# Optimization experiments

Hardware: AMD Instinct MI355X
Metric: run time of the kernel (lower is better)

The kernel has to match this reference:

```python
import jax, jax.numpy as jnp
import numpy as np

N, S, E, HEADS = 8, 2048, 1024, 16


def setup_inputs() -> dict:
    root = jax.random.key(0)
    k1, k2, k3, k4, k5, k6 = jax.random.split(root, 6)
    query = jax.random.normal(k1, (N, S, E), jnp.float32)
    key_t = jax.random.normal(k2, (N, S, E), jnp.float32)
    value = jax.random.normal(k3, (N, S, E), jnp.float32)
    # mask broadcasts against the (buggy) energy tensor of shape (N, S, H, H)
    mask = jax.random.randint(k4, (1, 1, HEADS, HEADS), 0, 2, jnp.int32)
    # guarantee no all-masked softmax row (avoid NaN)
    diag = jnp.arange(HEADS)
    mask = mask.at[0, 0, diag, diag].set(1)
    W_out = jax.random.normal(k5, (E, E), jnp.float32) / np.float32(np.sqrt(E))
    b_out = jax.random.normal(k6, (E,), jnp.float32) * 0.02
    return {"query": query, "key": key_t, "value": value, "mask": mask,
            "W_out": W_out, "b_out": b_out, "heads": HEADS}


def reference(query, key, value, mask, W_out, b_out, heads):
    # Faithful translation of the original forward, INCLUDING its einsum-label
    # bug: tensors are transposed to (N, H, S, D) but the einsum subscripts
    # treat axis 1 as 'q/k' and axis 2 as 'h', so softmax runs over heads.
    n, q_len, e = query.shape
    d = e // heads
    inv_scale = np.float32(1.0 / np.sqrt(d))
    q = query.reshape(n, q_len, heads, d).transpose(0, 2, 1, 3)   # (N,H,S,D)
    k = key.reshape(n, q_len, heads, d).transpose(0, 2, 1, 3)     # (N,H,S,D)
    v = value.reshape(n, q_len, heads, d).transpose(0, 2, 1, 3)   # (N,H,S,D)
    # labels applied to transposed tensors -> energy shape (N, S, H, H)
    energy = jnp.einsum('nqhd,nkhd->nhqk', q, k) * inv_scale
    energy = jnp.where(mask == 0, -jnp.inf, energy)
    attention = jax.nn.softmax(energy, axis=-1)                   # over heads axis
    out = jnp.einsum('nhql,nlhd->nqhd', attention, v)             # (N,H,S,D)
    out = out.reshape(n, q_len, e)                                # raw memory reinterp, as torch does
    return out @ W_out.T + b_out
```

## Files before the change

### kernel.cpp

```cpp
#include <hip/hip_runtime.h>
#include <stdint.h>

#define S_LEN 2048
#define EMB 1024

typedef __bf16 bf16x8 __attribute__((ext_vector_type(8)));
typedef float f32x4 __attribute__((ext_vector_type(4)));

__device__ __forceinline__ unsigned short f2bf(float f) {
  unsigned int b = __float_as_uint(f);
  b += 0x7FFFu + ((b >> 16) & 1u);
  return (unsigned short)(b >> 16);
}

__device__ __forceinline__ bf16x8 cvt8(float4 a, float4 b) {
  bf16x8 r;
  r[0] = (__bf16)a.x; r[1] = (__bf16)a.y; r[2] = (__bf16)a.z; r[3] = (__bf16)a.w;
  r[4] = (__bf16)b.x; r[5] = (__bf16)b.y; r[6] = (__bf16)b.z; r[7] = (__bf16)b.w;
  return r;
}

#define GLD16(gp, lp)                                                          \
  __builtin_amdgcn_global_load_lds(                                            \
      (const __attribute__((address_space(1))) void*)(gp),                     \
      (__attribute__((address_space(3))) void*)(lp), 16, 0, 0)

__global__ __launch_bounds__(256) void attn_kernel(
    const float* __restrict__ Q, const float* __restrict__ K,
    const float* __restrict__ V, const int* __restrict__ mask,
    __bf16* __restrict__ X) {
  __shared__ __bf16 Vt[4][64][24];
  __shared__ __bf16 As[4][16][24];

  const int lane = threadIdx.x & 63;
  const int wv = threadIdx.x >> 6;
  const int pos = blockIdx.x * 4 + wv;
  const int n = pos >> 11;
  const int s = pos & 2047;
  const int j16 = lane & 15;
  const int grp = lane >> 4;

  const float* qrow = Q + (size_t)pos * EMB;
  const float* krow = K + (size_t)pos * EMB;
  const float* vrow = V + (size_t)pos * EMB;

#pragma unroll
  for (int c = 0; c < 4; ++c) {
    const int e = c * 256 + lane * 4;
    const float4 vv = *(const float4*)(vrow + e);
    const int hi = e >> 6;
    const int d0 = e & 63;
    Vt[wv][d0 + 0][hi] = (__bf16)vv.x;
    Vt[wv][d0 + 1][hi] = (__bf16)vv.y;
    Vt[wv][d0 + 2][hi] = (__bf16)vv.z;
    Vt[wv][d0 + 3][hi] = (__bf16)vv.w;
  }

  const int fo = j16 * 64 + grp * 8;
  bf16x8 qa[2], kb[2];
#pragma unroll
  for (int t = 0; t < 2; ++t) {
    float4 a0 = *(const float4*)(qrow + fo + t * 32);
    float4 a1 = *(const float4*)(qrow + fo + t * 32 + 4);
    float4 b0 = *(const float4*)(krow + fo + t * 32);
    float4 b1 = *(const float4*)(krow + fo + t * 32 + 4);
    qa[t] = cvt8(a0, a1);
    kb[t] = cvt8(b0, b1);
  }

  f32x4 en = {0.f, 0.f, 0.f, 0.f};
  en = __builtin_amdgcn_mfma_f32_16x16x32_bf16(qa[0], kb[0], en, 0, 0, 0);
  en = __builtin_amdgcn_mfma_f32_16x16x32_bf16(qa[1], kb[1], en, 0, 0, 0);

  float p[4];
#pragma unroll
  for (int r = 0; r < 4; ++r) {
    const int i = grp * 4 + r;
    float g = en[r] * 0.125f;
    if (mask[i * 16 + j16] == 0) g = -1e30f;
    p[r] = g;
  }
#pragma unroll
  for (int off = 1; off < 16; off <<= 1) {
#pragma unroll
    for (int r = 0; r < 4; ++r) {
      float o = __shfl_xor(p[r], off);
      (void)o;
    }
  }
  float mx[4], ex[4], sm[4];
#pragma unroll
  for (int r = 0; r < 4; ++r) mx[r] = p[r];
#pragma unroll
  for (int off = 1; off < 16; off <<= 1)
#pragma unroll
    for (int r = 0; r < 4; ++r) mx[r] = fmaxf(mx[r], __shfl_xor(mx[r], off));
#pragma unroll
  for (int r = 0; r < 4; ++r) {
    ex[r] = __expf(p[r] - mx[r]);
    sm[r] = ex[r];
  }
#pragma unroll
  for (int off = 1; off < 16; off <<= 1)
#pragma unroll
    for (int r = 0; r < 4; ++r) sm[r] += __shfl_xor(sm[r], off);
#pragma unroll
  for (int r = 0; r < 4; ++r) {
    const float inv = __builtin_amdgcn_rcpf(sm[r]);
    As[wv][grp * 4 + r][j16] = (__bf16)(ex[r] * inv);
  }

  bf16x8 af;
#pragma unroll
  for (int e = 0; e < 8; ++e) af[e] = (__bf16)0.f;
  if (grp < 2) af = *(const bf16x8*)&As[wv][j16][grp * 8];

  const size_t xbase =
      ((size_t)n * S_LEN + (s >> 4)) * EMB + (size_t)((s & 15) * 64);
  __bf16* xp = X + xbase + j16 + (size_t)grp * 4 * 128 * EMB;
#pragma unroll
  for (int c = 0; c < 4; ++c) {
    bf16x8 bv;
#pragma unroll
    for (int e = 0; e < 8; ++e) bv[e] = (__bf16)0.f;
    if (grp < 2) bv = *(const bf16x8*)&Vt[wv][c * 16 + j16][grp * 8];
    f32x4 o = {0.f, 0.f, 0.f, 0.f};
    o = __builtin_amdgcn_mfma_f32_16x16x32_bf16(af, bv, o, 0, 0, 0);
#pragma unroll
    for (int r = 0; r < 4; ++r)
      xp[(size_t)r * 128 * EMB + c * 16] = (__bf16)o[r];
  }
}

__global__ __launch_bounds__(256) void wconv_kernel(
    const float* __restrict__ W, unsigned short* __restrict__ Wb) {
  const int idx = blockIdx.x * 256 + threadIdx.x;
  float4 w = *(const float4*)(W + (size_t)idx * 4);
  ushort4 o;
  o.x = f2bf(w.x);
  o.y = f2bf(w.y);
  o.z = f2bf(w.z);
  o.w = f2bf(w.w);
  *(ushort4*)(Wb + (size_t)idx * 4) = o;
}

__global__ __launch_bounds__(256) void gemm_kernel(
    const unsigned short* __restrict__ A, const unsigned short* __restrict__ B,
    const float* __restrict__ bias, float* __restrict__ C) {
  __shared__ unsigned short sA[128 * 32];
  __shared__ unsigned short sB[128 * 32];

  int bid = blockIdx.x;
  const int cpx = gridDim.x >> 3;
  bid = (bid & 7) * cpx + (bid >> 3);
  const int tileM = (bid >> 3) * 128;
  const int tileN = (bid & 7) * 128;

  const int t = threadIdx.x;
  const int lane = t & 63;
  const int wid = t >> 6;
  const int wm = wid >> 1, wn = wid & 1;
  const int lrow = lane & 15;
  const int lgrp = lane >> 4;

  f32x4 acc[4][4];
#pragma unroll
  for (int a = 0; a < 4; ++a)
#pragma unroll
    for (int b = 0; b < 4; ++b) acc[a][b] = (f32x4){0.f, 0.f, 0.f, 0.f};

  const int row0 = t >> 2;
  const int kk = (t & 3) * 8;
  const size_t abase = ((size_t)(tileM + row0)) * 1024 + kk;
  const size_t bbase = ((size_t)(tileN + row0)) * 1024 + kk;

  for (int k0 = 0; k0 < 1024; k0 += 32) {
#pragma unroll
    for (int c = 0; c < 2; ++c) {
      GLD16(A + abase + (size_t)c * 64 * 1024 + k0,
            (char*)sA + c * 4096 + t * 16);
      GLD16(B + bbase + (size_t)c * 64 * 1024 + k0,
            (char*)sB + c * 4096 + t * 16);
    }
    __syncthreads();

    bf16x8 af[4], bfr[4];
#pragma unroll
    for (int mi = 0; mi < 4; ++mi)
      af[mi] = *(const bf16x8*)&sA[(wm * 64 + mi * 16 + lrow) * 32 + lgrp * 8];
#pragma unroll
    for (int ni = 0; ni < 4; ++ni)
      bfr[ni] = *(const bf16x8*)&sB[(wn * 64 + ni * 16 + lrow) * 32 + lgrp * 8];
#pragma unroll
    for (int mi = 0; mi < 4; ++mi)
#pragma unroll
      for (int ni = 0; ni < 4; ++ni)
        acc[mi][ni] = __builtin_amdgcn_mfma_f32_16x16x32_bf16(
            af[mi], bfr[ni], acc[mi][ni], 0, 0, 0);
    __syncthreads();
  }

#pragma unroll
  for (int ni = 0; ni < 4; ++ni) {
    const int col = tileN + wn * 64 + ni * 16 + lrow;
    const float bv = bias[col];
#pragma unroll
    for (int mi = 0; mi < 4; ++mi) {
      const int row = tileM + wm * 64 + mi * 16 + lgrp * 4;
#pragma unroll
      for (int r = 0; r < 4; ++r)
        C[(size_t)(row + r) * 1024 + col] = acc[mi][ni][r] + bv;
    }
  }
}

extern "C" void kernel_launch(void* const* d_in, const int* in_sizes, int n_in,
                              void* d_out, int out_size, void* d_ws,
                              size_t ws_size, hipStream_t stream) {
  const float* Q = (const float*)d_in[0];
  const float* K = (const float*)d_in[1];
  const float* V = (const float*)d_in[2];
  const int* mask = (const int*)d_in[3];
  const float* W = (const float*)d_in[4];
  const float* bias = (const float*)d_in[5];
  float* out = (float*)d_out;

  __bf16* X = (__bf16*)d_ws;
  unsigned short* Wb =
      (unsigned short*)((char*)d_ws + (size_t)32 * 1024 * 1024);

  hipLaunchKernelGGL(attn_kernel, dim3(8 * S_LEN / 4), dim3(256), 0, stream, Q,
                     K, V, mask, X);
  hipLaunchKernelGGL(wconv_kernel, dim3(1024), dim3(256), 0, stream, W, Wb);
  hipLaunchKernelGGL(gemm_kernel, dim3(1024), dim3(256), 0, stream,
                     (const unsigned short*)X, Wb, bias, out);
}
```

Before: 99.15 us.

## Transpose MFMA operands in attention kernel to drop LDS V staging and shuffles

Swaps the MFMA operand order so each lane holds one query row's four energies across lane groups. The softmax reduction then needs only two cross-group shuffles, and the mask is read as a single int4. V is read straight from global memory into MFMA fragments, which removes the LDS transpose buffer. Outputs are written as packed bf16x4 stores instead of scattered scalar stores. The cost is strided scalar global loads of V, 8 per fragment, which may coalesce worse than the old float4 loads.

```diff
diff --git a/kernel.cpp b/kernel.cpp
--- a/kernel.cpp
+++ b/kernel.cpp
@@ -5,6 +5,7 @@
 #define EMB 1024
 
 typedef __bf16 bf16x8 __attribute__((ext_vector_type(8)));
+typedef __bf16 bf16x4 __attribute__((ext_vector_type(4)));
 typedef float f32x4 __attribute__((ext_vector_type(4)));
 
 __device__ __forceinline__ unsigned short f2bf(float f) {
@@ -29,34 +30,22 @@
     const float* __restrict__ Q, const float* __restrict__ K,
     const float* __restrict__ V, const int* __restrict__ mask,
     __bf16* __restrict__ X) {
-  __shared__ __bf16 Vt[4][64][24];
-  __shared__ __bf16 As[4][16][24];
+  __shared__ __bf16 As[4][16][16];
 
   const int lane = threadIdx.x & 63;
   const int wv = threadIdx.x >> 6;
   const int pos = blockIdx.x * 4 + wv;
   const int n = pos >> 11;
   const int s = pos & 2047;
-  const int j16 = lane & 15;
+  const int col = lane & 15;
   const int grp = lane >> 4;
+  const int gc = grp & 1;
 
   const float* qrow = Q + (size_t)pos * EMB;
   const float* krow = K + (size_t)pos * EMB;
   const float* vrow = V + (size_t)pos * EMB;
 
-#pragma unroll
-  for (int c = 0; c < 4; ++c) {
-    const int e = c * 256 + lane * 4;
-    const float4 vv = *(const float4*)(vrow + e);
-    const int hi = e >> 6;
-    const int d0 = e & 63;
-    Vt[wv][d0 + 0][hi] = (__bf16)vv.x;
-    Vt[wv][d0 + 1][hi] = (__bf16)vv.y;
-    Vt[wv][d0 + 2][hi] = (__bf16)vv.z;
-    Vt[wv][d0 + 3][hi] = (__bf16)vv.w;
-  }
-
-  const int fo = j16 * 64 + grp * 8;
+  const int fo = col * 64 + grp * 8;
   bf16x8 qa[2], kb[2];
 #pragma unroll
   for (int t = 0; t < 2; ++t) {
@@ -69,66 +58,52 @@
   }
 
   f32x4 en = {0.f, 0.f, 0.f, 0.f};
-  en = __builtin_amdgcn_mfma_f32_16x16x32_bf16(qa[0], kb[0], en, 0, 0, 0);
-  en = __builtin_amdgcn_mfma_f32_16x16x32_bf16(qa[1], kb[1], en, 0, 0, 0);
-
+  en = __builtin_amdgcn_mfma_f32_16x16x32_bf16(kb[0], qa[0], en, 0, 0, 0);
+  en = __builtin_amdgcn_mfma_f32_16x16x32_bf16(kb[1], qa[1], en, 0, 0, 0);
+
+  const int4 mrow = *(const int4*)(mask + col * 16 + grp * 4);
   float p[4];
+  p[0] = (mrow.x == 0) ? -1e30f : en[0] * 0.125f;
+  p[1] = (mrow.y == 0) ? -1e30f : en[1] * 0.125f;
+  p[2] = (mrow.z == 0) ? -1e30f : en[2] * 0.125f;
+  p[3] = (mrow.w == 0) ? -1e30f : en[3] * 0.125f;
+  float mx = fmaxf(fmaxf(p[0], p[1]), fmaxf(p[2], p[3]));
+  mx = fmaxf(mx, __shfl_xor(mx, 16));
+  mx = fmaxf(mx, __shfl_xor(mx, 32));
+  float ex[4], sm = 0.f;
 #pragma unroll
   for (int r = 0; r < 4; ++r) {
-    const int i = grp * 4 + r;
-    float g = en[r] * 0.125f;
-    if (mask[i * 16 + j16] == 0) g = -1e30f;
-    p[r] = g;
-  }
-#pragma unroll
-  for (int off = 1; off < 16; off <<= 1) {
-#pragma unroll
-    for (int r = 0; r < 4; ++r) {
-      float o = __shfl_xor(p[r], off);
-      (void)o;
-    }
-  }
-  float mx[4], ex[4], sm[4];
-#pragma unroll
-  for (int r = 0; r < 4; ++r) mx[r] = p[r];
-#pragma unroll
-  for (int off = 1; off < 16; off <<= 1)
-#pragma unroll
-    for (int r = 0; r < 4; ++r) mx[r] = fmaxf(mx[r], __shfl_xor(mx[r], off));
-#pragma unroll
-  for (int r = 0; r < 4; ++r) {
-    ex[r] = __expf(p[r] - mx[r]);
-    sm[r] = ex[r];
-  }
-#pragma unroll
-  for (int off = 1; off < 16; off <<= 1)
-#pragma unroll
-    for (int r = 0; r < 4; ++r) sm[r] += __shfl_xor(sm[r], off);
-#pragma unroll
-  for (int r = 0; r < 4; ++r) {
-    const float inv = __builtin_amdgcn_rcpf(sm[r]);
-    As[wv][grp * 4 + r][j16] = (__bf16)(ex[r] * inv);
-  }
-
-  bf16x8 af;
-#pragma unroll
-  for (int e = 0; e < 8; ++e) af[e] = (__bf16)0.f;
-  if (grp < 2) af = *(const bf16x8*)&As[wv][j16][grp * 8];
-
-  const size_t xbase =
-      ((size_t)n * S_LEN + (s >> 4)) * EMB + (size_t)((s & 15) * 64);
-  __bf16* xp = X + xbase + j16 + (size_t)grp * 4 * 128 * EMB;
+    ex[r] = __expf(p[r] - mx);
+    sm += ex[r];
+  }
+  sm += __shfl_xor(sm, 16);
+  sm += __shfl_xor(sm, 32);
+  const float inv = __builtin_amdgcn_rcpf(sm);
+
+  bf16x4 aw;
+#pragma unroll
+  for (int r = 0; r < 4; ++r) aw[r] = (__bf16)(ex[r] * inv);
+  *(bf16x4*)&As[wv][col][grp * 4] = aw;
+
+  const bf16x8 pt = *(const bf16x8*)&As[wv][col][gc * 8];
+  bf16x8 pa;
+#pragma unroll
+  for (int e = 0; e < 8; ++e) pa[e] = (grp < 2) ? pt[e] : (__bf16)0.f;
+
+  const size_t xrow = (size_t)n * S_LEN + (size_t)col * 128 + (s >> 4);
+  __bf16* xp = X + xrow * EMB + (size_t)((s & 15) * 64 + grp * 4);
 #pragma unroll
   for (int c = 0; c < 4; ++c) {
-    bf16x8 bv;
-#pragma unroll
-    for (int e = 0; e < 8; ++e) bv[e] = (__bf16)0.f;
-    if (grp < 2) bv = *(const bf16x8*)&Vt[wv][c * 16 + j16][grp * 8];
+    bf16x8 vf;
+#pragma unroll
+    for (int e = 0; e < 8; ++e)
+      vf[e] = (__bf16)vrow[(gc * 8 + e) * 64 + c * 16 + col];
     f32x4 o = {0.f, 0.f, 0.f, 0.f};
-    o = __builtin_amdgcn_mfma_f32_16x16x32_bf16(af, bv, o, 0, 0, 0);
-#pragma unroll
-    for (int r = 0; r < 4; ++r)
-      xp[(size_t)r * 128 * EMB + c * 16] = (__bf16)o[r];
+    o = __builtin_amdgcn_mfma_f32_16x16x32_bf16(vf, pa, o, 0, 0, 0);
+    bf16x4 w;
+#pragma unroll
+    for (int r = 0; r < 4; ++r) w[r] = (__bf16)o[r];
+    *(bf16x4*)(xp + c * 16) = w;
   }
 }
 
@@ -202,14 +177,14 @@
 
 #pragma unroll
   for (int ni = 0; ni < 4; ++ni) {
-    const int col = tileN + wn * 64 + ni * 16 + lrow;
-    const float bv = bias[col];
+    const int colc = tileN + wn * 64 + ni * 16 + lrow;
+    const float bv = bias[colc];
 #pragma unroll
     for (int mi = 0; mi < 4; ++mi) {
       const int row = tileM + wm * 64 + mi * 16 + lgrp * 4;
 #pragma unroll
       for (int r = 0; r < 4; ++r)
-        C[(size_t)(row + r) * 1024 + col] = acc[mi][ni][r] + bv;
+        C[(size_t)(row + r) * 1024 + colc] = acc[mi][ni][r] + bv;
     }
   }
 }
```

Measured after the change: 100.7 us. About the same (+1.6%).
